# Kernel tuning notes

Hardware: AMD Instinct MI355X
Metric: run time of the kernel (lower is better)

## Reference

```python
import jax, jax.numpy as jnp
import numpy as np

B, N, L, D_IN, D = 32, 2048, 32768, 4, 64


def setup_inputs() -> dict:
    key = jax.random.key(0)
    ks = jax.random.split(key, 10)
    s = 0.05  # modest init scale for params
    return {
        "pred_node": jax.random.normal(ks[0], (B, N, D_IN), jnp.float32),
        "line_param": jax.random.normal(ks[1], (B, L, 4), jnp.float32),
        "W_embed": jax.random.normal(ks[2], (D_IN, D), jnp.float32) * s,
        "b_embed": jnp.zeros((D,), jnp.float32),
        "W1": jax.random.normal(ks[3], (2 * D, D), jnp.float32) * s,
        "b1": jnp.zeros((D,), jnp.float32),
        "W2": jax.random.normal(ks[4], (D, 4), jnp.float32) * s,
        "b2": jnp.zeros((4,), jnp.float32),
        "edge_src": jax.random.randint(ks[5], (B, L), 0, N, jnp.int32),
        "edge_dst": jax.random.randint(ks[6], (B, L), 0, N, jnp.int32),
    }


def reference(pred_node, line_param, W_embed, b_embed, W1, b1, W2, b2,
              edge_src, edge_dst):
    # node_feat_to_line_feat: Linear(4 -> d_model) over all nodes at once
    node_feat = jnp.einsum("bni,id->bnd", pred_node, W_embed) + b_embed  # (B,N,D)

    # Batched gather of node-feature pairs per edge (replaces Python loops)
    fi = jnp.take_along_axis(node_feat, edge_src[..., None].astype(jnp.int32), axis=1)  # (B,L,D)
    fj = jnp.take_along_axis(node_feat, edge_dst[..., None].astype(jnp.int32), axis=1)  # (B,L,D)
    combined = jnp.concatenate([fi, fj], axis=-1)  # (B,L,2D)

    # line_pred_head: Linear(2D->D) -> ReLU -> Dropout(eval: identity) -> Linear(D->4)
    h = jax.nn.relu(jnp.einsum("ble,ed->bld", combined, W1) + b1)
    line_pred = jnp.einsum("bld,do->blo", h, W2) + b2  # (B,L,4)

    # Cols 0,1 copied from line_param; cols 2,3 from the prediction head
    out = jnp.concatenate([line_param[..., :2], line_pred[..., 2:4]], axis=-1)
    return out
```

## Files before the change

### kernel.cpp

```cpp
#include <hip/hip_runtime.h>
#include <hip/hip_fp16.h>
#include <stdint.h>

#define B_ 32
#define N_ 2048
#define L_ 32768


static __device__ __forceinline__ __half2 pkrtz(float a, float b) {
    return __float22half2_rn(make_float2(a, b));
}

static __device__ __forceinline__ __half2 pkmax(__half2 a, __half2 b) {
    __half2 r;
    asm("v_pk_max_f16 %0, %1, %2" : "=v"(r) : "v"(a), "v"(b));
    return r;
}

__global__ __launch_bounds__(512) void prep_kernel(
    const float* __restrict__ W_embed, const float* __restrict__ b_embed,
    const float* __restrict__ W1, const float* __restrict__ b1,
    const float* __restrict__ W2, __half2* __restrict__ wh) {
    __shared__ float sacc[64][8];
    __shared__ float sbias[64];
    int tid = threadIdx.x;
    int d = tid & 63;
    int i = (tid >> 6) & 3;
    int half_ = tid >> 8;

    const float* w1base = W1 + (half_ ? 64 * 64 : 0);
    float acc = 0.f;
#pragma unroll
    for (int k = 0; k < 64; ++k) {
        acc = fmaf(W_embed[i * 64 + k], w1base[k * 64 + d], acc);
    }
    sacc[d][half_ * 4 + i] = acc;

    if (tid < 64) {
        float bb = 0.f;
#pragma unroll
        for (int k = 0; k < 64; ++k) {
            bb = fmaf(b_embed[k], W1[k * 64 + d] + W1[(64 + k) * 64 + d], bb);
        }
        sbias[d] = bb + b1[d];
    }
    __syncthreads();

    if (tid < 64) {
#pragma unroll
        for (int k = 0; k < 8; ++k) {
            float v = sacc[tid][k];
            wh[tid * 12 + k] = pkrtz(v, v);
        }
        float bv = sbias[tid];
        wh[tid * 12 + 8] = pkrtz(bv, bv);
        float c2 = W2[tid * 4 + 2];
        float c3 = W2[tid * 4 + 3];
        wh[tid * 12 + 9] = pkrtz(c2, c2);
        wh[tid * 12 + 10] = pkrtz(c3, c3);
        wh[tid * 12 + 11] = pkrtz(0.f, 0.f);
    }
}

__global__ __launch_bounds__(256, 4) void edge_kernel(
    const float4* __restrict__ pred_node,
    const __half2* __restrict__ wh,
    const int* __restrict__ esrc, const int* __restrict__ edst,
    const float2* __restrict__ lp2,
    const float* __restrict__ b2,
    float4* __restrict__ out) {
    __shared__ float4 spn[N_];

    int tid = threadIdx.x;
    int bid = blockIdx.x;
    int x = bid & 7;
    int i = bid >> 3;
    int b = x + 8 * (i >> 5);
    int j = i & 31;

    const float4* pnb = pred_node + b * N_;
#pragma unroll
    for (int q = 0; q < 8; ++q) {
        int idx = tid + q * 256;
        spn[idx] = pnb[idx];
    }

    int ebase = b * L_ + j * 1024 + tid;

    int sa[4], ta[4];
#pragma unroll
    for (int p = 0; p < 4; ++p) {
        int e = ebase + p * 256;
        sa[p] = esrc[e];
        ta[p] = edst[e];
    }
    float bias2 = b2[2], bias3 = b2[3];

    __syncthreads();

    __half2 px[2][8];
#pragma unroll
    for (int pr = 0; pr < 2; ++pr) {
        float4 s0 = spn[sa[2 * pr]];
        float4 s1 = spn[sa[2 * pr + 1]];
        float4 t0 = spn[ta[2 * pr]];
        float4 t1 = spn[ta[2 * pr + 1]];
        px[pr][0] = pkrtz(s0.x, s1.x);
        px[pr][1] = pkrtz(s0.y, s1.y);
        px[pr][2] = pkrtz(s0.z, s1.z);
        px[pr][3] = pkrtz(s0.w, s1.w);
        px[pr][4] = pkrtz(t0.x, t1.x);
        px[pr][5] = pkrtz(t0.y, t1.y);
        px[pr][6] = pkrtz(t0.z, t1.z);
        px[pr][7] = pkrtz(t0.w, t1.w);
    }

    const __half2 zero = pkrtz(0.f, 0.f);
    __half2 acc2[2] = {zero, zero};
    __half2 acc3[2] = {zero, zero};

#pragma unroll 4
    for (int f = 0; f < 64; ++f) {
        const __half2* wf = wh + f * 12;
        __half2 w0 = wf[0], w1 = wf[1], w2w = wf[2], w3w = wf[3];
        __half2 w4 = wf[4], w5 = wf[5], w6w = wf[6], w7w = wf[7];
        __half2 bs = wf[8];
        __half2 c2 = wf[9], c3 = wf[10];
#pragma unroll
        for (int pr = 0; pr < 2; ++pr) {
            __half2 h = bs;
            h = __hfma2(px[pr][0], w0, h);
            h = __hfma2(px[pr][1], w1, h);
            h = __hfma2(px[pr][2], w2w, h);
            h = __hfma2(px[pr][3], w3w, h);
            h = __hfma2(px[pr][4], w4, h);
            h = __hfma2(px[pr][5], w5, h);
            h = __hfma2(px[pr][6], w6w, h);
            h = __hfma2(px[pr][7], w7w, h);
            h = pkmax(h, zero);
            acc2[pr] = __hfma2(h, c2, acc2[pr]);
            acc3[pr] = __hfma2(h, c3, acc3[pr]);
        }
    }

#pragma unroll
    for (int p = 0; p < 4; ++p) {
        int e = ebase + p * 256;
        float2 lp = lp2[(size_t)e * 2];
        int pr = p >> 1;
        float r2 = (p & 1) ? __high2float(acc2[pr]) : __low2float(acc2[pr]);
        float r3 = (p & 1) ? __high2float(acc3[pr]) : __low2float(acc3[pr]);
        out[e] = make_float4(lp.x, lp.y, bias2 + r2, bias3 + r3);
    }
}

extern "C" void kernel_launch(void* const* d_in, const int* in_sizes, int n_in,
                              void* d_out, int out_size, void* d_ws, size_t ws_size,
                              hipStream_t stream) {
    const float* pred_node = (const float*)d_in[0];
    const float* line_param = (const float*)d_in[1];
    const float* W_embed = (const float*)d_in[2];
    const float* b_embed = (const float*)d_in[3];
    const float* W1 = (const float*)d_in[4];
    const float* b1 = (const float*)d_in[5];
    const float* W2 = (const float*)d_in[6];
    const float* b2 = (const float*)d_in[7];
    const int* esrc = (const int*)d_in[8];
    const int* edst = (const int*)d_in[9];
    float* out = (float*)d_out;

    __half2* wh = (__half2*)d_ws;

    prep_kernel<<<1, 512, 0, stream>>>(W_embed, b_embed, W1, b1, W2, wh);
    edge_kernel<<<1024, 256, 0, stream>>>((const float4*)pred_node, wh,
                                          esrc, edst,
                                          (const float2*)line_param, b2,
                                          (float4*)out);
}
```

Before: 106.0 us.

## Fuse weight-folding prep into edge kernel and stage folded weights in LDS

Removes the separate single-block prep kernel. Each block now recomputes the folded W_embed·W1 weights, bias and W2 columns into shared memory. The edge loop then reads them as vectorized float4 LDS loads instead of global half2 loads. This drops a kernel launch and the serial dependency between the two kernels, at the cost of redundant per-block weight computation (64-iteration loops reading W1 from global/L2) before the main work.

New measurement: 156.1 us. 47.3% more time.

```diff
diff --git a/kernel.cpp b/kernel.cpp
--- a/kernel.cpp
+++ b/kernel.cpp
@@ -17,59 +17,22 @@
     return r;
 }
 
-__global__ __launch_bounds__(512) void prep_kernel(
+static __device__ __forceinline__ __half2 bits_h2(float x) {
+    union { float f; __half2 h; } u;
+    u.f = x;
+    return u.h;
+}
+
+__global__ __launch_bounds__(256, 4) void fused_kernel(
+    const float4* __restrict__ pred_node,
     const float* __restrict__ W_embed, const float* __restrict__ b_embed,
     const float* __restrict__ W1, const float* __restrict__ b1,
-    const float* __restrict__ W2, __half2* __restrict__ wh) {
-    __shared__ float sacc[64][8];
-    __shared__ float sbias[64];
-    int tid = threadIdx.x;
-    int d = tid & 63;
-    int i = (tid >> 6) & 3;
-    int half_ = tid >> 8;
-
-    const float* w1base = W1 + (half_ ? 64 * 64 : 0);
-    float acc = 0.f;
-#pragma unroll
-    for (int k = 0; k < 64; ++k) {
-        acc = fmaf(W_embed[i * 64 + k], w1base[k * 64 + d], acc);
-    }
-    sacc[d][half_ * 4 + i] = acc;
-
-    if (tid < 64) {
-        float bb = 0.f;
-#pragma unroll
-        for (int k = 0; k < 64; ++k) {
-            bb = fmaf(b_embed[k], W1[k * 64 + d] + W1[(64 + k) * 64 + d], bb);
-        }
-        sbias[d] = bb + b1[d];
-    }
-    __syncthreads();
-
-    if (tid < 64) {
-#pragma unroll
-        for (int k = 0; k < 8; ++k) {
-            float v = sacc[tid][k];
-            wh[tid * 12 + k] = pkrtz(v, v);
-        }
-        float bv = sbias[tid];
-        wh[tid * 12 + 8] = pkrtz(bv, bv);
-        float c2 = W2[tid * 4 + 2];
-        float c3 = W2[tid * 4 + 3];
-        wh[tid * 12 + 9] = pkrtz(c2, c2);
-        wh[tid * 12 + 10] = pkrtz(c3, c3);
-        wh[tid * 12 + 11] = pkrtz(0.f, 0.f);
-    }
-}
-
-__global__ __launch_bounds__(256, 4) void edge_kernel(
-    const float4* __restrict__ pred_node,
-    const __half2* __restrict__ wh,
+    const float* __restrict__ W2, const float* __restrict__ b2,
     const int* __restrict__ esrc, const int* __restrict__ edst,
     const float2* __restrict__ lp2,
-    const float* __restrict__ b2,
     float4* __restrict__ out) {
     __shared__ float4 spn[N_];
+    __shared__ __align__(16) __half2 swh[64 * 12];
 
     int tid = threadIdx.x;
     int bid = blockIdx.x;
@@ -77,13 +40,6 @@
     int i = bid >> 3;
     int b = x + 8 * (i >> 5);
     int j = i & 31;
-
-    const float4* pnb = pred_node + b * N_;
-#pragma unroll
-    for (int q = 0; q < 8; ++q) {
-        int idx = tid + q * 256;
-        spn[idx] = pnb[idx];
-    }
 
     int ebase = b * L_ + j * 1024 + tid;
 
@@ -94,6 +50,43 @@
         sa[p] = esrc[e];
         ta[p] = edst[e];
     }
+
+    const float4* pnb = pred_node + b * N_;
+#pragma unroll
+    for (int q = 0; q < 8; ++q) {
+        int idx = tid + q * 256;
+        spn[idx] = pnb[idx];
+    }
+
+    {
+        int f = tid & 63;
+        int g = tid >> 6;
+        float acc_t = 0.f, acc_b = 0.f, acc_bias = 0.f;
+#pragma unroll
+        for (int k = 0; k < 64; ++k) {
+            float wt = W1[k * 64 + f];
+            float wb = W1[(64 + k) * 64 + f];
+            float we = W_embed[g * 64 + k];
+            acc_t = fmaf(we, wt, acc_t);
+            acc_b = fmaf(we, wb, acc_b);
+            if (g == 0) acc_bias = fmaf(b_embed[k], wt + wb, acc_bias);
+        }
+        swh[f * 12 + g] = pkrtz(acc_t, acc_t);
+        swh[f * 12 + 4 + g] = pkrtz(acc_b, acc_b);
+        if (g == 0) {
+            float bv = acc_bias + b1[f];
+            swh[f * 12 + 8] = pkrtz(bv, bv);
+        } else if (g == 1) {
+            float c2 = W2[f * 4 + 2];
+            swh[f * 12 + 9] = pkrtz(c2, c2);
+        } else if (g == 2) {
+            float c3 = W2[f * 4 + 3];
+            swh[f * 12 + 10] = pkrtz(c3, c3);
+        } else {
+            swh[f * 12 + 11] = pkrtz(0.f, 0.f);
+        }
+    }
+
     float bias2 = b2[2], bias3 = b2[3];
 
     __syncthreads();
@@ -121,11 +114,14 @@
 
 #pragma unroll 4
     for (int f = 0; f < 64; ++f) {
-        const __half2* wf = wh + f * 12;
-        __half2 w0 = wf[0], w1 = wf[1], w2w = wf[2], w3w = wf[3];
-        __half2 w4 = wf[4], w5 = wf[5], w6w = wf[6], w7w = wf[7];
-        __half2 bs = wf[8];
-        __half2 c2 = wf[9], c3 = wf[10];
+        const float4* wv = reinterpret_cast<const float4*>(swh) + f * 3;
+        float4 q0 = wv[0], q1 = wv[1], q2 = wv[2];
+        __half2 w0 = bits_h2(q0.x), w1 = bits_h2(q0.y);
+        __half2 w2w = bits_h2(q0.z), w3w = bits_h2(q0.w);
+        __half2 w4 = bits_h2(q1.x), w5 = bits_h2(q1.y);
+        __half2 w6w = bits_h2(q1.z), w7w = bits_h2(q1.w);
+        __half2 bs = bits_h2(q2.x);
+        __half2 c2 = bits_h2(q2.y), c3 = bits_h2(q2.z);
 #pragma unroll
         for (int pr = 0; pr < 2; ++pr) {
             __half2 h = bs;
@@ -169,11 +165,9 @@
     const int* edst = (const int*)d_in[9];
     float* out = (float*)d_out;
 
-    __half2* wh = (__half2*)d_ws;
-
-    prep_kernel<<<1, 512, 0, stream>>>(W_embed, b_embed, W1, b1, W2, wh);
-    edge_kernel<<<1024, 256, 0, stream>>>((const float4*)pred_node, wh,
-                                          esrc, edst,
-                                          (const float2*)line_param, b2,
-                                          (float4*)out);
+    fused_kernel<<<1024, 256, 0, stream>>>((const float4*)pred_node,
+                                           W_embed, b_embed, W1, b1, W2, b2,
+                                           esrc, edst,
+                                           (const float2*)line_param,
+                                           (float4*)out);
 }
```

## Gather node features directly from global memory and halve edges per thread

Applied to the files above, without the earlier changes.

Drops the shared-memory staging of each batch's node table and gathers the four needed node rows per thread straight from global (L2-cached) memory. It also halves the edges per thread from 4 to 2, doubles the grid to 2048 blocks and raises the occupancy hint to 8. This removes the 32 KB-per-block staging load and the block barrier, trading them for random global gathers and less per-thread amortisation of the weight loads.

Measured after the change: 107.7 us. About the same (+1.6%).

```diff
diff --git a/kernel.cpp b/kernel.cpp
--- a/kernel.cpp
+++ b/kernel.cpp
@@ -62,62 +62,42 @@
     }
 }
 
-__global__ __launch_bounds__(256, 4) void edge_kernel(
+__global__ __launch_bounds__(256, 8) void edge_kernel(
     const float4* __restrict__ pred_node,
     const __half2* __restrict__ wh,
     const int* __restrict__ esrc, const int* __restrict__ edst,
     const float2* __restrict__ lp2,
     const float* __restrict__ b2,
     float4* __restrict__ out) {
-    __shared__ float4 spn[N_];
-
     int tid = threadIdx.x;
     int bid = blockIdx.x;
     int x = bid & 7;
     int i = bid >> 3;
-    int b = x + 8 * (i >> 5);
-    int j = i & 31;
+    int b = x + 8 * (i >> 6);
+    int j = i & 63;
+
+    int ebase = b * L_ + j * 512 + tid;
+
+    int s0 = esrc[ebase], s1 = esrc[ebase + 256];
+    int t0 = edst[ebase], t1 = edst[ebase + 256];
 
     const float4* pnb = pred_node + b * N_;
-#pragma unroll
-    for (int q = 0; q < 8; ++q) {
-        int idx = tid + q * 256;
-        spn[idx] = pnb[idx];
-    }
+    float4 vs0 = pnb[s0];
+    float4 vs1 = pnb[s1];
+    float4 vt0 = pnb[t0];
+    float4 vt1 = pnb[t1];
 
-    int ebase = b * L_ + j * 1024 + tid;
-
-    int sa[4], ta[4];
-#pragma unroll
-    for (int p = 0; p < 4; ++p) {
-        int e = ebase + p * 256;
-        sa[p] = esrc[e];
-        ta[p] = edst[e];
-    }
-    float bias2 = b2[2], bias3 = b2[3];
-
-    __syncthreads();
-
-    __half2 px[2][8];
-#pragma unroll
-    for (int pr = 0; pr < 2; ++pr) {
-        float4 s0 = spn[sa[2 * pr]];
-        float4 s1 = spn[sa[2 * pr + 1]];
-        float4 t0 = spn[ta[2 * pr]];
-        float4 t1 = spn[ta[2 * pr + 1]];
-        px[pr][0] = pkrtz(s0.x, s1.x);
-        px[pr][1] = pkrtz(s0.y, s1.y);
-        px[pr][2] = pkrtz(s0.z, s1.z);
-        px[pr][3] = pkrtz(s0.w, s1.w);
-        px[pr][4] = pkrtz(t0.x, t1.x);
-        px[pr][5] = pkrtz(t0.y, t1.y);
-        px[pr][6] = pkrtz(t0.z, t1.z);
-        px[pr][7] = pkrtz(t0.w, t1.w);
-    }
+    __half2 px0 = pkrtz(vs0.x, vs1.x);
+    __half2 px1 = pkrtz(vs0.y, vs1.y);
+    __half2 px2 = pkrtz(vs0.z, vs1.z);
+    __half2 px3 = pkrtz(vs0.w, vs1.w);
+    __half2 px4 = pkrtz(vt0.x, vt1.x);
+    __half2 px5 = pkrtz(vt0.y, vt1.y);
+    __half2 px6 = pkrtz(vt0.z, vt1.z);
+    __half2 px7 = pkrtz(vt0.w, vt1.w);
 
     const __half2 zero = pkrtz(0.f, 0.f);
-    __half2 acc2[2] = {zero, zero};
-    __half2 acc3[2] = {zero, zero};
+    __half2 acc2 = zero, acc3 = zero;
 
 #pragma unroll 4
     for (int f = 0; f < 64; ++f) {
@@ -126,32 +106,29 @@
         __half2 w4 = wf[4], w5 = wf[5], w6w = wf[6], w7w = wf[7];
         __half2 bs = wf[8];
         __half2 c2 = wf[9], c3 = wf[10];
-#pragma unroll
-        for (int pr = 0; pr < 2; ++pr) {
-            __half2 h = bs;
-            h = __hfma2(px[pr][0], w0, h);
-            h = __hfma2(px[pr][1], w1, h);
-            h = __hfma2(px[pr][2], w2w, h);
-            h = __hfma2(px[pr][3], w3w, h);
-            h = __hfma2(px[pr][4], w4, h);
-            h = __hfma2(px[pr][5], w5, h);
-            h = __hfma2(px[pr][6], w6w, h);
-            h = __hfma2(px[pr][7], w7w, h);
-            h = pkmax(h, zero);
-            acc2[pr] = __hfma2(h, c2, acc2[pr]);
-            acc3[pr] = __hfma2(h, c3, acc3[pr]);
-        }
+        __half2 h = bs;
+        h = __hfma2(px0, w0, h);
+        h = __hfma2(px1, w1, h);
+        h = __hfma2(px2, w2w, h);
+        h = __hfma2(px3, w3w, h);
+        h = __hfma2(px4, w4, h);
+        h = __hfma2(px5, w5, h);
+        h = __hfma2(px6, w6w, h);
+        h = __hfma2(px7, w7w, h);
+        h = pkmax(h, zero);
+        acc2 = __hfma2(h, c2, acc2);
+        acc3 = __hfma2(h, c3, acc3);
     }
 
-#pragma unroll
-    for (int p = 0; p < 4; ++p) {
-        int e = ebase + p * 256;
-        float2 lp = lp2[(size_t)e * 2];
-        int pr = p >> 1;
-        float r2 = (p & 1) ? __high2float(acc2[pr]) : __low2float(acc2[pr]);
-        float r3 = (p & 1) ? __high2float(acc3[pr]) : __low2float(acc3[pr]);
-        out[e] = make_float4(lp.x, lp.y, bias2 + r2, bias3 + r3);
-    }
+    float bias2 = b2[2], bias3 = b2[3];
+    float2 lp0 = lp2[(size_t)ebase * 2];
+    float2 lp1 = lp2[(size_t)(ebase + 256) * 2];
+    out[ebase] = make_float4(lp0.x, lp0.y,
+                             bias2 + __low2float(acc2),
+                             bias3 + __low2float(acc3));
+    out[ebase + 256] = make_float4(lp1.x, lp1.y,
+                                   bias2 + __high2float(acc2),
+                                   bias3 + __high2float(acc3));
 }
 
 extern "C" void kernel_launch(void* const* d_in, const int* in_sizes, int n_in,
@@ -172,7 +149,7 @@
     __half2* wh = (__half2*)d_ws;
 
     prep_kernel<<<1, 512, 0, stream>>>(W_embed, b_embed, W1, b1, W2, wh);
-    edge_kernel<<<1024, 256, 0, stream>>>((const float4*)pred_node, wh,
+    edge_kernel<<<2048, 256, 0, stream>>>((const float4*)pred_node, wh,
                                           esrc, edst,
                                           (const float2*)line_param, b2,
                                           (float4*)out);
```

## Gather node features directly from global memory instead of staging in LDS

Applied to the files above, without the earlier changes.

Removes the per-block LDS staging of the whole pred_node batch slice (32KB per block, repeated by 32 blocks per batch) and the barrier, gathering node features straight from global/L2 instead. The launch bound's occupancy hint rises from 4 to 8 blocks, the 64-iteration hidden loop is fully unrolled, and the weights are read as 128-bit vector loads. line_param is now read as float4 rows rather than strided float2. The catch is that random global gathers have higher latency than LDS reads, plus more register pressure from the full unroll.

New measurement: 109.4 us. 1.03x slower.

```diff
diff --git a/kernel.cpp b/kernel.cpp
--- a/kernel.cpp
+++ b/kernel.cpp
@@ -7,7 +7,7 @@
 #define L_ 32768
 
 
-static __device__ __forceinline__ __half2 pkrtz(float a, float b) {
+static __device__ __forceinline__ __half2 pkrn(float a, float b) {
     return __float22half2_rn(make_float2(a, b));
 }
 
@@ -15,6 +15,12 @@
     __half2 r;
     asm("v_pk_max_f16 %0, %1, %2" : "=v"(r) : "v"(a), "v"(b));
     return r;
+}
+
+static __device__ __forceinline__ __half2 bits_h2(float x) {
+    union { float f; __half2 h; } u;
+    u.f = x;
+    return u.h;
 }
 
 __global__ __launch_bounds__(512) void prep_kernel(
@@ -50,82 +56,72 @@
 #pragma unroll
         for (int k = 0; k < 8; ++k) {
             float v = sacc[tid][k];
-            wh[tid * 12 + k] = pkrtz(v, v);
+            wh[tid * 12 + k] = pkrn(v, v);
         }
         float bv = sbias[tid];
-        wh[tid * 12 + 8] = pkrtz(bv, bv);
+        wh[tid * 12 + 8] = pkrn(bv, bv);
         float c2 = W2[tid * 4 + 2];
         float c3 = W2[tid * 4 + 3];
-        wh[tid * 12 + 9] = pkrtz(c2, c2);
-        wh[tid * 12 + 10] = pkrtz(c3, c3);
-        wh[tid * 12 + 11] = pkrtz(0.f, 0.f);
+        wh[tid * 12 + 9] = pkrn(c2, c2);
+        wh[tid * 12 + 10] = pkrn(c3, c3);
+        wh[tid * 12 + 11] = pkrn(0.f, 0.f);
     }
 }
 
-__global__ __launch_bounds__(256, 4) void edge_kernel(
+__global__ __launch_bounds__(256, 8) void edge_kernel(
     const float4* __restrict__ pred_node,
     const __half2* __restrict__ wh,
     const int* __restrict__ esrc, const int* __restrict__ edst,
-    const float2* __restrict__ lp2,
+    const float4* __restrict__ lp4,
     const float* __restrict__ b2,
     float4* __restrict__ out) {
-    __shared__ float4 spn[N_];
-
-    int tid = threadIdx.x;
-    int bid = blockIdx.x;
-    int x = bid & 7;
-    int i = bid >> 3;
-    int b = x + 8 * (i >> 5);
-    int j = i & 31;
-
-    const float4* pnb = pred_node + b * N_;
-#pragma unroll
-    for (int q = 0; q < 8; ++q) {
-        int idx = tid + q * 256;
-        spn[idx] = pnb[idx];
-    }
-
-    int ebase = b * L_ + j * 1024 + tid;
+    const int tid = threadIdx.x;
+    const int bid = blockIdx.x;
+    const int x = bid & 7;
+    const int i = bid >> 3;
+    const int b = x + 8 * (i >> 5);
+    const int j = i & 31;
+    const int ebase = b * L_ + j * 1024 + tid;
 
     int sa[4], ta[4];
 #pragma unroll
     for (int p = 0; p < 4; ++p) {
-        int e = ebase + p * 256;
-        sa[p] = esrc[e];
-        ta[p] = edst[e];
+        sa[p] = esrc[ebase + p * 256];
+        ta[p] = edst[ebase + p * 256];
     }
-    float bias2 = b2[2], bias3 = b2[3];
 
-    __syncthreads();
-
+    const float4* pnb = pred_node + b * N_;
     __half2 px[2][8];
 #pragma unroll
     for (int pr = 0; pr < 2; ++pr) {
-        float4 s0 = spn[sa[2 * pr]];
-        float4 s1 = spn[sa[2 * pr + 1]];
-        float4 t0 = spn[ta[2 * pr]];
-        float4 t1 = spn[ta[2 * pr + 1]];
-        px[pr][0] = pkrtz(s0.x, s1.x);
-        px[pr][1] = pkrtz(s0.y, s1.y);
-        px[pr][2] = pkrtz(s0.z, s1.z);
-        px[pr][3] = pkrtz(s0.w, s1.w);
-        px[pr][4] = pkrtz(t0.x, t1.x);
-        px[pr][5] = pkrtz(t0.y, t1.y);
-        px[pr][6] = pkrtz(t0.z, t1.z);
-        px[pr][7] = pkrtz(t0.w, t1.w);
+        float4 s0 = pnb[sa[2 * pr]];
+        float4 s1 = pnb[sa[2 * pr + 1]];
+        float4 t0 = pnb[ta[2 * pr]];
+        float4 t1 = pnb[ta[2 * pr + 1]];
+        px[pr][0] = pkrn(s0.x, s1.x);
+        px[pr][1] = pkrn(s0.y, s1.y);
+        px[pr][2] = pkrn(s0.z, s1.z);
+        px[pr][3] = pkrn(s0.w, s1.w);
+        px[pr][4] = pkrn(t0.x, t1.x);
+        px[pr][5] = pkrn(t0.y, t1.y);
+        px[pr][6] = pkrn(t0.z, t1.z);
+        px[pr][7] = pkrn(t0.w, t1.w);
     }
 
-    const __half2 zero = pkrtz(0.f, 0.f);
+    const __half2 zero = pkrn(0.f, 0.f);
     __half2 acc2[2] = {zero, zero};
     __half2 acc3[2] = {zero, zero};
 
-#pragma unroll 4
+#pragma unroll
     for (int f = 0; f < 64; ++f) {
-        const __half2* wf = wh + f * 12;
-        __half2 w0 = wf[0], w1 = wf[1], w2w = wf[2], w3w = wf[3];
-        __half2 w4 = wf[4], w5 = wf[5], w6w = wf[6], w7w = wf[7];
-        __half2 bs = wf[8];
-        __half2 c2 = wf[9], c3 = wf[10];
+        const float4* wv = reinterpret_cast<const float4*>(wh) + f * 3;
+        float4 q0 = wv[0], q1 = wv[1], q2 = wv[2];
+        __half2 w0 = bits_h2(q0.x), w1 = bits_h2(q0.y);
+        __half2 w2w = bits_h2(q0.z), w3w = bits_h2(q0.w);
+        __half2 w4 = bits_h2(q1.x), w5 = bits_h2(q1.y);
+        __half2 w6w = bits_h2(q1.z), w7w = bits_h2(q1.w);
+        __half2 bs = bits_h2(q2.x);
+        __half2 c2 = bits_h2(q2.y), c3 = bits_h2(q2.z);
 #pragma unroll
         for (int pr = 0; pr < 2; ++pr) {
             __half2 h = bs;
@@ -143,10 +139,11 @@
         }
     }
 
+    float bias2 = b2[2], bias3 = b2[3];
 #pragma unroll
     for (int p = 0; p < 4; ++p) {
         int e = ebase + p * 256;
-        float2 lp = lp2[(size_t)e * 2];
+        float4 lp = lp4[e];
         int pr = p >> 1;
         float r2 = (p & 1) ? __high2float(acc2[pr]) : __low2float(acc2[pr]);
         float r3 = (p & 1) ? __high2float(acc3[pr]) : __low2float(acc3[pr]);
@@ -174,6 +171,6 @@
     prep_kernel<<<1, 512, 0, stream>>>(W_embed, b_embed, W1, b1, W2, wh);
     edge_kernel<<<1024, 256, 0, stream>>>((const float4*)pred_node, wh,
                                           esrc, edst,
-                                          (const float2*)line_param, b2,
+                                          (const float4*)line_param, b2,
                                           (float4*)out);
 }
```
